# Performance work log

Hardware: AMD Instinct MI355X
Metric: run time of the kernel (lower is better)

The kernel has to match this reference:

```python
import jax, jax.numpy as jnp
import numpy as np

B, NQ, NK = 16, 512, 1024
CQ, CV = 128, 128
H, D = 8, 64            # nb_heads, attention_size
SCALE = float(np.sqrt(D))


def setup_inputs() -> dict:
    key = jax.random.key(0)
    ks = jax.random.split(key, 10)
    s = 0.02
    return {
        "query": jax.random.normal(ks[0], (B, NQ, CQ), jnp.float32),
        "key": jax.random.normal(ks[1], (B, NK, CV), jnp.float32),
        "c_mask": jax.random.randint(ks[2], (B, NK), 0, 2).astype(jnp.float32),
        # torch Linear params, stored as [in, out] so y = x @ W + b
        "Wq": jax.random.normal(ks[3], (CQ, H * D), jnp.float32) * s,
        "bq": jnp.zeros((H * D,), jnp.float32),
        "Wk": jax.random.normal(ks[4], (CV, H * D), jnp.float32) * s,
        "bk": jnp.zeros((H * D,), jnp.float32),
        "Wv": jax.random.normal(ks[5], (CV, H * D), jnp.float32) * s,
        "bv": jnp.zeros((H * D,), jnp.float32),
    }


def reference(query, key, c_mask, Wq, bq, Wk, bk, Wv, bv):
    # projections -> [B, N, H, D]
    q = (query @ Wq + bq).reshape(B, NQ, H, D)
    k = (key @ Wk + bk).reshape(B, NK, H, D)
    v = (key @ Wv + bv).reshape(B, NK, H, D)
    # scaled scores [B, H, NQ, NK]
    scores = jnp.einsum('bqhd,bkhd->bhqk', q / SCALE, k)
    # additive mask: c_mask [B, NK] broadcasts over heads and queries
    scores = scores - 100000.0 * (1.0 - c_mask[:, None, None, :])
    attn = jax.nn.softmax(scores, axis=-1)
    # weighted values -> [B, NQ, H, D] -> concat heads
    c = jnp.einsum('bhqk,bkhd->bqhd', attn, v)
    return c.reshape(B, NQ, H * D)
```

## Files before the change

kernel.cpp:

```cpp
#include <hip/hip_runtime.h>
#include <hip/hip_bf16.h>

#define B_  16
#define NQ_ 512
#define NK_ 1024
#define CQ_ 128
#define H_  8
#define D_  64
#define HD_ 512

typedef __attribute__((ext_vector_type(8))) short short8;
typedef __attribute__((ext_vector_type(4))) float floatx4;

__device__ __forceinline__ short f2bf(float f) {
    union { float f; unsigned u; } x; x.f = f;
    unsigned r = (x.u + 0x7fffu + ((x.u >> 16) & 1u)) >> 16;
    return (short)r;
}
__device__ __forceinline__ int f2bf_pk(float a, float b) {
    __hip_bfloat162 h = __float22bfloat162_rn(make_float2(a, b));
    int r; __builtin_memcpy(&r, &h, 4); return r;
}
__device__ __forceinline__ short8 pack8(float4 a, float4 b) {
    union { int4 i; short8 s; } u;
    u.i = make_int4(f2bf_pk(a.x, a.y), f2bf_pk(a.z, a.w),
                    f2bf_pk(b.x, b.y), f2bf_pk(b.z, b.w));
    return u.s;
}
__device__ __forceinline__ int2 packi2(floatx4 a) {
    return make_int2(f2bf_pk(a[0], a[1]), f2bf_pk(a[2], a[3]));
}
__device__ __forceinline__ void async16(const short* g, short* l) {
    __builtin_amdgcn_global_load_lds(
        (const __attribute__((address_space(1))) void*)g,
        (__attribute__((address_space(3))) void*)l, 16, 0, 0);
}

__global__ __launch_bounds__(256) void prep_kernel(
    const float* __restrict__ W0, const float* __restrict__ W1,
    const float* __restrict__ W2, short* __restrict__ T0,
    short* __restrict__ T1, short* __restrict__ T2,
    const float* __restrict__ bq, float* __restrict__ bqs, float qscale,
    const float* __restrict__ cmask, int* __restrict__ idx,
    float* __restrict__ cm2, int* __restrict__ npad)
{
    const int blk = blockIdx.x, t = threadIdx.x;
    if (blk == 48) {
        bqs[t]       = bq[t] * qscale;
        bqs[t + 256] = bq[t + 256] * qscale;
        return;
    }
    if (blk >= 49) {
        __shared__ int wsum[4];
        const int b = blk - 49;
        const int w = t >> 6, lane = t & 63;
        float4 m4 = *(const float4*)(cmask + b * NK_ + t * 4);
        const int m0 = m4.x > 0.5f, m1 = m4.y > 0.5f, m2 = m4.z > 0.5f, m3 = m4.w > 0.5f;
        const int s = m0 + m1 + m2 + m3;
        int v = s;
        #pragma unroll
        for (int off = 1; off < 64; off <<= 1) {
            int u = __shfl_up(v, off);
            if (lane >= off) v += u;
        }
        if (lane == 63) wsum[w] = v;
        __syncthreads();
        int pre = 0;
        #pragma unroll
        for (int i = 0; i < 4; ++i) if (i < w) pre += wsum[i];
        int pos = pre + v - s;
        const int base = b * NK_;
        if (m0) { idx[base + pos] = t * 4 + 0; cm2[base + pos] = 1.0f; ++pos; }
        if (m1) { idx[base + pos] = t * 4 + 1; cm2[base + pos] = 1.0f; ++pos; }
        if (m2) { idx[base + pos] = t * 4 + 2; cm2[base + pos] = 1.0f; ++pos; }
        if (m3) { idx[base + pos] = t * 4 + 3; cm2[base + pos] = 1.0f; ++pos; }
        const int total = wsum[0] + wsum[1] + wsum[2] + wsum[3];
        for (int j = total + t; j < NK_; j += 256) {
            idx[base + j] = 0; cm2[base + j] = 0.0f;
        }
        if (t == 0) npad[b] = (total + 127) & ~127;
        return;
    }
    __shared__ short tsh[32 * 132];
    const int mat = blk >> 4, nb = blk & 15;
    const float* W = mat == 0 ? W0 : (mat == 1 ? W1 : W2);
    short* T = mat == 0 ? T0 : (mat == 1 ? T1 : T2);
    const float s = mat == 0 ? qscale : 1.0f;
    #pragma unroll
    for (int i = 0; i < 4; ++i) {
        const int i2 = i * 256 + t;
        const int k = i2 >> 3, c = (i2 & 7) * 4;
        float4 v = *(const float4*)(W + (size_t)k * HD_ + nb * 32 + c);
        tsh[(c + 0) * 132 + k] = f2bf(v.x * s);
        tsh[(c + 1) * 132 + k] = f2bf(v.y * s);
        tsh[(c + 2) * 132 + k] = f2bf(v.z * s);
        tsh[(c + 3) * 132 + k] = f2bf(v.w * s);
    }
    __syncthreads();
    #pragma unroll
    for (int j = 0; j < 2; ++j) {
        const int i2 = j * 256 + t;
        const int n = i2 >> 4, seg = (i2 & 15) * 8;
        *(short8*)(T + (size_t)(nb * 32 + n) * CQ_ + seg) =
            *(const short8*)&tsh[n * 132 + seg];
    }
}

__global__ __launch_bounds__(256, 4) void kvproj_kernel(
    const float* __restrict__ key_,
    const short* __restrict__ wkt, const short* __restrict__ wvt,
    const float* __restrict__ bk, const float* __restrict__ bv,
    short* __restrict__ ks, short* __restrict__ vt,
    const int* __restrict__ idx, const int* __restrict__ npad)
{
    __shared__ __align__(16) short csh[9216];

    int bx = blockIdx.x;
    const short* Wt; const float* bias; short* out; int transposed;
    if (bx < 128) { Wt = wkt; bias = bk; out = ks; transposed = 0; }
    else { bx -= 128; Wt = wvt; bias = bv; out = vt; transposed = 1; }

    const int mbase = bx * 128;
    const int b  = mbase >> 10;
    const int r0 = mbase & 1023;
    if (r0 >= npad[b]) return;

    const int tid  = threadIdx.x;
    const int w    = tid >> 6, lane = tid & 63;
    const int l15  = lane & 15, quad = lane >> 4;
    const int* ib = idx + b * NK_;

    short8 afr[2][4];
    #pragma unroll
    for (int mt = 0; mt < 2; ++mt) {
        const int krow = ib[r0 + w * 32 + mt * 16 + l15];
        const float* xrow = key_ + (size_t)(b * NK_ + krow) * CQ_;
        #pragma unroll
        for (int kt = 0; kt < 4; ++kt)
            afr[mt][kt] = pack8(*(const float4*)(xrow + kt * 32 + quad * 8),
                                *(const float4*)(xrow + kt * 32 + quad * 8 + 4));
    }

    #pragma unroll
    for (int hh = 0; hh < 2; ++hh) {
        const int h = blockIdx.y * 2 + hh;
        short8 bfr[4][4];
        #pragma unroll
        for (int nt = 0; nt < 4; ++nt) {
            const short8* wrow = (const short8*)(Wt + (size_t)(h * 64 + nt * 16 + l15) * CQ_);
            #pragma unroll
            for (int kt = 0; kt < 4; ++kt) bfr[nt][kt] = wrow[kt * 4 + quad];
        }
        floatx4 acc[2][4];
        #pragma unroll
        for (int mt = 0; mt < 2; ++mt)
            #pragma unroll
            for (int nt = 0; nt < 4; ++nt) {
                floatx4 a = {0.f, 0.f, 0.f, 0.f};
                #pragma unroll
                for (int kt = 0; kt < 4; ++kt)
                    a = __builtin_amdgcn_mfma_f32_16x16x32_bf16(afr[mt][kt], bfr[nt][kt], a, 0, 0, 0);
                acc[mt][nt] = a;
            }
        __syncthreads();
        #pragma unroll
        for (int mt = 0; mt < 2; ++mt)
            #pragma unroll
            for (int nt = 0; nt < 4; ++nt) {
                const float bvv = bias[h * 64 + nt * 16 + l15];
                #pragma unroll
                for (int i = 0; i < 4; ++i) {
                    const short s = f2bf(acc[mt][nt][i] + bvv);
                    const int m = w * 32 + mt * 16 + quad * 4 + i;
                    const int n = nt * 16 + l15;
                    if (!transposed) csh[m * 72 + n]  = s;
                    else             csh[n * 136 + m] = s;
                }
            }
        __syncthreads();

        const size_t bh = (size_t)(b * H_ + h);
        if (!transposed) {
            short* dst = out + (bh * NK_ + r0) * D_;
            #pragma unroll
            for (int it = 0; it < 4; ++it) {
                const int i2 = it * 256 + tid;
                const int row = i2 >> 3, c8 = (i2 & 7) * 8;
                *(short8*)(dst + i2 * 8) = *(const short8*)&csh[row * 72 + c8];
            }
        } else {
            short* dst = out + bh * D_ * NK_ + r0;
            #pragma unroll
            for (int it = 0; it < 4; ++it) {
                const int i2 = it * 256 + tid;
                const int row = i2 >> 4, c8 = (i2 & 15) * 8;
                *(short8*)(dst + (size_t)row * NK_ + c8) = *(const short8*)&csh[row * 136 + c8];
            }
        }
    }
}

__global__ __launch_bounds__(256, 4) void attn_kernel(
    const float* __restrict__ query, const short* __restrict__ ks,
    const short* __restrict__ vt, const float* __restrict__ cm2,
    const short* __restrict__ wqt, const float* __restrict__ bqs,
    const int* __restrict__ npad, float* __restrict__ out)
{
    __shared__ __align__(16) short kbuf[2][64 * 64];
    __shared__ __align__(16) short vbuf[2][64 * 64];
    __shared__ __align__(16) short psh[64 * 64];

    const int tid = threadIdx.x;
    const int w = tid >> 6, lane = tid & 63;
    const int l15 = lane & 15, quad = lane >> 4;

    const int bx   = blockIdx.x;
    const int bh_i = bx & 127;
    const int qq   = bx >> 7;
    const int h    = bh_i & 7;
    const int b    = bh_i >> 3;

    const size_t bh = (size_t)bh_i;
    const short* kb_ = ks + bh * NK_ * D_;
    const short* vb  = vt + bh * D_ * NK_;
    const float* mk  = cm2 + (size_t)b * NK_;
    const int nc = npad[b] >> 6;

    const int prow = w * 16 + l15;

    short8 qa[2];
    {
        short8 waf[4][4];
        #pragma unroll
        for (int dt = 0; dt < 4; ++dt)
            #pragma unroll
            for (int kt = 0; kt < 4; ++kt)
                waf[dt][kt] = *(const short8*)(wqt + (size_t)(h * 64 + dt * 16 + l15) * CQ_ + kt * 32 + quad * 8);
        const float* qrow = query + ((size_t)b * NQ_ + qq * 64 + prow) * CQ_;
        short8 bqf[4];
        #pragma unroll
        for (int kt = 0; kt < 4; ++kt)
            bqf[kt] = pack8(*(const float4*)(qrow + kt * 32 + quad * 8),
                            *(const float4*)(qrow + kt * 32 + quad * 8 + 4));
        #pragma unroll
        for (int dt = 0; dt < 4; ++dt) {
            float4 bi = *(const float4*)(bqs + h * 64 + dt * 16 + quad * 4);
            floatx4 a = {bi.x, bi.y, bi.z, bi.w};
            #pragma unroll
            for (int kt = 0; kt < 4; ++kt)
                a = __builtin_amdgcn_mfma_f32_16x16x32_bf16(waf[dt][kt], bqf[kt], a, 0, 0, 0);
            const int c16 = (dt * 2 + (quad >> 1)) ^ (prow & 7);
            *(int2*)&psh[prow * 64 + c16 * 8 + (quad & 1) * 4] = packi2(a);
        }
        qa[0] = *(const short8*)&psh[prow * 64 + ((quad    ) ^ (prow & 7)) * 8];
        qa[1] = *(const short8*)&psh[prow * 64 + ((4 + quad) ^ (prow & 7)) * 8];
    }

    const int srow8 = lane >> 3, sc = lane & 7;
    auto stage = [&](int kb0, short* kdst, short* vdst) {
        #pragma unroll
        for (int j = 0; j < 2; ++j) {
            const int row = w * 16 + j * 8 + srow8;
            const int cs = sc ^ (row & 7);
            async16(kb_ + (size_t)(kb0 + row) * D_ + cs * 8, &kdst[(w * 16 + j * 8) * 64]);
            async16(vb + (size_t)row * NK_ + kb0 + cs * 8, &vdst[(w * 16 + j * 8) * 64]);
        }
    };

    float l_lane = 0.f;
    floatx4 o_acc[4];
    #pragma unroll
    for (int dt = 0; dt < 4; ++dt) o_acc[dt] = (floatx4){0.f, 0.f, 0.f, 0.f};

    stage(0, kbuf[0], vbuf[0]);
    __syncthreads();

    for (int t = 0; t < nc; ++t) {
        const int cur = t & 1;
        if (t + 1 < nc) stage((t + 1) * 64, kbuf[cur ^ 1], vbuf[cur ^ 1]);
        const short* kb  = kbuf[cur];
        const short* vbl = vbuf[cur];
        const int kbase = t * 64;

        short8 ka[4][2];
        #pragma unroll
        for (int nt = 0; nt < 4; ++nt) {
            const int row = nt * 16 + l15;
            ka[nt][0] = *(const short8*)&kb[row * 64 + ((quad    ) ^ (row & 7)) * 8];
            ka[nt][1] = *(const short8*)&kb[row * 64 + ((4 + quad) ^ (row & 7)) * 8];
        }
        short8 vf[2][4];
        #pragma unroll
        for (int dt = 0; dt < 4; ++dt) {
            const int row = dt * 16 + l15;
            vf[0][dt] = *(const short8*)&vbl[row * 64 + ((quad    ) ^ (row & 7)) * 8];
            vf[1][dt] = *(const short8*)&vbl[row * 64 + ((4 + quad) ^ (row & 7)) * 8];
        }
        float4 m4[4];
        #pragma unroll
        for (int nt = 0; nt < 4; ++nt)
            m4[nt] = *(const float4*)(mk + kbase + nt * 16 + quad * 4);

        floatx4 st[4];
        #pragma unroll
        for (int nt = 0; nt < 4; ++nt) {
            floatx4 a = {0.f, 0.f, 0.f, 0.f};
            a = __builtin_amdgcn_mfma_f32_16x16x32_bf16(ka[nt][1], qa[1], a, 0, 0, 0);
            a = __builtin_amdgcn_mfma_f32_16x16x32_bf16(ka[nt][0], qa[0], a, 0, 0, 0);
            st[nt] = a;
        }
        float psum = 0.f;
        #pragma unroll
        for (int nt = 0; nt < 4; ++nt) {
            float p0 = m4[nt].x * __builtin_amdgcn_exp2f(st[nt][0]);
            float p1 = m4[nt].y * __builtin_amdgcn_exp2f(st[nt][1]);
            float p2 = m4[nt].z * __builtin_amdgcn_exp2f(st[nt][2]);
            float p3 = m4[nt].w * __builtin_amdgcn_exp2f(st[nt][3]);
            psum += (p0 + p1) + (p2 + p3);
            int2 pk = make_int2(f2bf_pk(p0, p1), f2bf_pk(p2, p3));
            const int c16 = (2 * nt + (quad >> 1)) ^ (prow & 7);
            *(int2*)&psh[prow * 64 + c16 * 8 + (quad & 1) * 4] = pk;
        }
        l_lane += psum;
        #pragma unroll
        for (int kt = 0; kt < 2; ++kt) {
            short8 pa = *(const short8*)&psh[prow * 64 + ((kt * 4 + quad) ^ (prow & 7)) * 8];
            #pragma unroll
            for (int dt = 0; dt < 4; ++dt)
                o_acc[dt] = __builtin_amdgcn_mfma_f32_16x16x32_bf16(vf[kt][dt], pa, o_acc[dt], 0, 0, 0);
        }
        __syncthreads();
    }

    {
        float ls = l_lane;
        ls += __shfl_xor(ls, 16);
        ls += __shfl_xor(ls, 32);
        const float linv = 1.0f / ls;
        const int qr = qq * 64 + prow;
        float* orow = out + ((size_t)b * NQ_ + qr) * HD_ + h * D_;
        #pragma unroll
        for (int dt = 0; dt < 4; ++dt) {
            float4 v = make_float4(o_acc[dt][0] * linv, o_acc[dt][1] * linv,
                                   o_acc[dt][2] * linv, o_acc[dt][3] * linv);
            *(float4*)(orow + dt * 16 + quad * 4) = v;
        }
    }
}

extern "C" void kernel_launch(void* const* d_in, const int* in_sizes, int n_in,
                              void* d_out, int out_size, void* d_ws, size_t ws_size,
                              hipStream_t stream) {
    const float* query = (const float*)d_in[0];
    const float* key   = (const float*)d_in[1];
    const float* cmask = (const float*)d_in[2];
    const float* Wq    = (const float*)d_in[3];
    const float* bq    = (const float*)d_in[4];
    const float* Wk    = (const float*)d_in[5];
    const float* bk    = (const float*)d_in[6];
    const float* Wv    = (const float*)d_in[7];
    const float* bv    = (const float*)d_in[8];
    float* out = (float*)d_out;

    char* ws = (char*)d_ws;
    short* ks  = (short*)(ws);
    short* vt  = (short*)(ws + (size_t)(16u << 20));
    char*  w32 = ws + (size_t)(32u << 20);
    short* wqt = (short*)(w32);
    short* wkt = (short*)(w32 + 131072);
    short* wvt = (short*)(w32 + 131072 * 2);
    float* bqs = (float*)(w32 + 131072 * 3);
    int*   idx = (int*)(w32 + 131072 * 3 + 4096);
    float* cm2 = (float*)(w32 + 131072 * 3 + 4096 + 65536);
    int*  npad = (int*)(w32 + 131072 * 3 + 4096 + 131072);

    const float qscale = 0.125f * 1.44269504f;
    prep_kernel<<<dim3(65), dim3(256), 0, stream>>>(
        Wq, Wk, Wv, wqt, wkt, wvt, bq, bqs, qscale, cmask, idx, cm2, npad);

    kvproj_kernel<<<dim3(256, 4), dim3(256), 0, stream>>>(
        key, wkt, wvt, bk, bv, ks, vt, idx, npad);

    attn_kernel<<<dim3(1024), dim3(256), 0, stream>>>(
        query, ks, vt, cm2, wqt, bqs, npad, out);
}
```

Before: 139.7 us.

## Fuse K/V projection and attention into one kernel with atomic-flag dependencies

Result: slower. 222.9 us (+59.6%).

```diff
diff --git a/kernel.cpp b/kernel.cpp
--- a/kernel.cpp
+++ b/kernel.cpp
@@ -106,244 +106,260 @@
     }
 }
 
-__global__ __launch_bounds__(256, 4) void kvproj_kernel(
-    const float* __restrict__ key_,
-    const short* __restrict__ wkt, const short* __restrict__ wvt,
-    const float* __restrict__ bk, const float* __restrict__ bv,
-    short* __restrict__ ks, short* __restrict__ vt,
-    const int* __restrict__ idx, const int* __restrict__ npad)
+__global__ __launch_bounds__(256, 4) void kvattn_kernel(
+    const float* __restrict__ query, const float* __restrict__ key_,
+    const short* __restrict__ wqt, const short* __restrict__ wkt,
+    const short* __restrict__ wvt, const float* __restrict__ bk,
+    const float* __restrict__ bv, const float* __restrict__ bqs,
+    const int* __restrict__ idx, const float* __restrict__ cm2,
+    const int* __restrict__ npad, short* __restrict__ ks,
+    short* __restrict__ vt, unsigned* __restrict__ flags,
+    float* __restrict__ out)
 {
-    __shared__ __align__(16) short csh[9216];
-
-    int bx = blockIdx.x;
-    const short* Wt; const float* bias; short* out; int transposed;
-    if (bx < 128) { Wt = wkt; bias = bk; out = ks; transposed = 0; }
-    else { bx -= 128; Wt = wvt; bias = bv; out = vt; transposed = 1; }
-
-    const int mbase = bx * 128;
-    const int b  = mbase >> 10;
-    const int r0 = mbase & 1023;
-    if (r0 >= npad[b]) return;
-
-    const int tid  = threadIdx.x;
-    const int w    = tid >> 6, lane = tid & 63;
-    const int l15  = lane & 15, quad = lane >> 4;
-    const int* ib = idx + b * NK_;
-
-    short8 afr[2][4];
-    #pragma unroll
-    for (int mt = 0; mt < 2; ++mt) {
-        const int krow = ib[r0 + w * 32 + mt * 16 + l15];
-        const float* xrow = key_ + (size_t)(b * NK_ + krow) * CQ_;
-        #pragma unroll
-        for (int kt = 0; kt < 4; ++kt)
-            afr[mt][kt] = pack8(*(const float4*)(xrow + kt * 32 + quad * 8),
-                                *(const float4*)(xrow + kt * 32 + quad * 8 + 4));
-    }
-
-    #pragma unroll
-    for (int hh = 0; hh < 2; ++hh) {
-        const int h = blockIdx.y * 2 + hh;
-        short8 bfr[4][4];
-        #pragma unroll
-        for (int nt = 0; nt < 4; ++nt) {
-            const short8* wrow = (const short8*)(Wt + (size_t)(h * 64 + nt * 16 + l15) * CQ_);
-            #pragma unroll
-            for (int kt = 0; kt < 4; ++kt) bfr[nt][kt] = wrow[kt * 4 + quad];
-        }
-        floatx4 acc[2][4];
-        #pragma unroll
-        for (int mt = 0; mt < 2; ++mt)
-            #pragma unroll
-            for (int nt = 0; nt < 4; ++nt) {
-                floatx4 a = {0.f, 0.f, 0.f, 0.f};
-                #pragma unroll
-                for (int kt = 0; kt < 4; ++kt)
-                    a = __builtin_amdgcn_mfma_f32_16x16x32_bf16(afr[mt][kt], bfr[nt][kt], a, 0, 0, 0);
-                acc[mt][nt] = a;
-            }
-        __syncthreads();
-        #pragma unroll
-        for (int mt = 0; mt < 2; ++mt)
-            #pragma unroll
-            for (int nt = 0; nt < 4; ++nt) {
-                const float bvv = bias[h * 64 + nt * 16 + l15];
-                #pragma unroll
-                for (int i = 0; i < 4; ++i) {
-                    const short s = f2bf(acc[mt][nt][i] + bvv);
-                    const int m = w * 32 + mt * 16 + quad * 4 + i;
-                    const int n = nt * 16 + l15;
-                    if (!transposed) csh[m * 72 + n]  = s;
-                    else             csh[n * 136 + m] = s;
-                }
-            }
-        __syncthreads();
-
-        const size_t bh = (size_t)(b * H_ + h);
-        if (!transposed) {
-            short* dst = out + (bh * NK_ + r0) * D_;
-            #pragma unroll
-            for (int it = 0; it < 4; ++it) {
-                const int i2 = it * 256 + tid;
-                const int row = i2 >> 3, c8 = (i2 & 7) * 8;
-                *(short8*)(dst + i2 * 8) = *(const short8*)&csh[row * 72 + c8];
-            }
-        } else {
-            short* dst = out + bh * D_ * NK_ + r0;
-            #pragma unroll
-            for (int it = 0; it < 4; ++it) {
-                const int i2 = it * 256 + tid;
-                const int row = i2 >> 4, c8 = (i2 & 15) * 8;
-                *(short8*)(dst + (size_t)row * NK_ + c8) = *(const short8*)&csh[row * 136 + c8];
-            }
-        }
-    }
-}
-
-__global__ __launch_bounds__(256, 4) void attn_kernel(
-    const float* __restrict__ query, const short* __restrict__ ks,
-    const short* __restrict__ vt, const float* __restrict__ cm2,
-    const short* __restrict__ wqt, const float* __restrict__ bqs,
-    const int* __restrict__ npad, float* __restrict__ out)
-{
-    __shared__ __align__(16) short kbuf[2][64 * 64];
-    __shared__ __align__(16) short vbuf[2][64 * 64];
-    __shared__ __align__(16) short psh[64 * 64];
-
+    __shared__ __align__(16) char smem[40960];
     const int tid = threadIdx.x;
     const int w = tid >> 6, lane = tid & 63;
     const int l15 = lane & 15, quad = lane >> 4;
 
-    const int bx   = blockIdx.x;
-    const int bh_i = bx & 127;
-    const int qq   = bx >> 7;
-    const int h    = bh_i & 7;
-    const int b    = bh_i >> 3;
-
-    const size_t bh = (size_t)bh_i;
-    const short* kb_ = ks + bh * NK_ * D_;
-    const short* vb  = vt + bh * D_ * NK_;
-    const float* mk  = cm2 + (size_t)b * NK_;
-    const int nc = npad[b] >> 6;
-
-    const int prow = w * 16 + l15;
-
-    short8 qa[2];
     {
-        short8 waf[4][4];
+        int bx = blockIdx.x & 255;
+        const int y = blockIdx.x >> 8;
+        const short* Wt; const float* bias; short* op; int transposed;
+        if (bx < 128) { Wt = wkt; bias = bk; op = ks; transposed = 0; }
+        else { bx -= 128; Wt = wvt; bias = bv; op = vt; transposed = 1; }
+
+        const int mbase = bx * 128;
+        const int b  = mbase >> 10;
+        const int r0 = mbase & 1023;
+        if (r0 < npad[b]) {
+            short* csh = (short*)smem;
+            const int* ib = idx + b * NK_;
+
+            short8 afr[2][4];
+            #pragma unroll
+            for (int mt = 0; mt < 2; ++mt) {
+                const int krow = ib[r0 + w * 32 + mt * 16 + l15];
+                const float* xrow = key_ + (size_t)(b * NK_ + krow) * CQ_;
+                #pragma unroll
+                for (int kt = 0; kt < 4; ++kt)
+                    afr[mt][kt] = pack8(*(const float4*)(xrow + kt * 32 + quad * 8),
+                                        *(const float4*)(xrow + kt * 32 + quad * 8 + 4));
+            }
+
+            #pragma unroll
+            for (int hh = 0; hh < 2; ++hh) {
+                const int h = y * 2 + hh;
+                short8 bfr[4][4];
+                #pragma unroll
+                for (int nt = 0; nt < 4; ++nt) {
+                    const short8* wrow = (const short8*)(Wt + (size_t)(h * 64 + nt * 16 + l15) * CQ_);
+                    #pragma unroll
+                    for (int kt = 0; kt < 4; ++kt) bfr[nt][kt] = wrow[kt * 4 + quad];
+                }
+                floatx4 acc[2][4];
+                #pragma unroll
+                for (int mt = 0; mt < 2; ++mt)
+                    #pragma unroll
+                    for (int nt = 0; nt < 4; ++nt) {
+                        floatx4 a = {0.f, 0.f, 0.f, 0.f};
+                        #pragma unroll
+                        for (int kt = 0; kt < 4; ++kt)
+                            a = __builtin_amdgcn_mfma_f32_16x16x32_bf16(afr[mt][kt], bfr[nt][kt], a, 0, 0, 0);
+                        acc[mt][nt] = a;
+                    }
+                __syncthreads();
+                #pragma unroll
+                for (int mt = 0; mt < 2; ++mt)
+                    #pragma unroll
+                    for (int nt = 0; nt < 4; ++nt) {
+                        const float bvv = bias[h * 64 + nt * 16 + l15];
+                        #pragma unroll
+                        for (int i = 0; i < 4; ++i) {
+                            const short sv = f2bf(acc[mt][nt][i] + bvv);
+                            const int m = w * 32 + mt * 16 + quad * 4 + i;
+                            const int n = nt * 16 + l15;
+                            if (!transposed) csh[m * 72 + n]  = sv;
+                            else             csh[n * 136 + m] = sv;
+                        }
+                    }
+                __syncthreads();
+
+                const size_t bh = (size_t)(b * H_ + h);
+                if (!transposed) {
+                    short* dst = op + (bh * NK_ + r0) * D_;
+                    #pragma unroll
+                    for (int it = 0; it < 4; ++it) {
+                        const int i2 = it * 256 + tid;
+                        const int row = i2 >> 3, c8 = (i2 & 7) * 8;
+                        *(short8*)(dst + i2 * 8) = *(const short8*)&csh[row * 72 + c8];
+                    }
+                } else {
+                    short* dst = op + bh * D_ * NK_ + r0;
+                    #pragma unroll
+                    for (int it = 0; it < 4; ++it) {
+                        const int i2 = it * 256 + tid;
+                        const int row = i2 >> 4, c8 = (i2 & 15) * 8;
+                        *(short8*)(dst + (size_t)row * NK_ + c8) = *(const short8*)&csh[row * 136 + c8];
+                    }
+                }
+            }
+            __syncthreads();
+        }
+        if (tid == 0) {
+            __threadfence();
+            atomicAdd(&flags[(b * 4 + y) * 2 + transposed], 1u);
+        }
+    }
+
+    {
+        short* const kbuf0 = (short*)smem;
+        short* const vbuf0 = (short*)smem + 8192;
+        short* const psh   = (short*)smem + 16384;
+
+        const int bx   = blockIdx.x;
+        const int bh_i = bx & 127;
+        const int qq   = bx >> 7;
+        const int h    = bh_i & 7;
+        const int b    = bh_i >> 3;
+
+        const size_t bh = (size_t)bh_i;
+        const short* kb_ = ks + bh * NK_ * D_;
+        const short* vb  = vt + bh * D_ * NK_;
+        const float* mk  = cm2 + (size_t)b * NK_;
+        const int nc = npad[b] >> 6;
+
+        const int prow = w * 16 + l15;
+
+        short8 qa[2];
+        {
+            short8 waf[4][4];
+            #pragma unroll
+            for (int dt = 0; dt < 4; ++dt)
+                #pragma unroll
+                for (int kt = 0; kt < 4; ++kt)
+                    waf[dt][kt] = *(const short8*)(wqt + (size_t)(h * 64 + dt * 16 + l15) * CQ_ + kt * 32 + quad * 8);
+            const float* qrow = query + ((size_t)b * NQ_ + qq * 64 + prow) * CQ_;
+            short8 bqf[4];
+            #pragma unroll
+            for (int kt = 0; kt < 4; ++kt)
+                bqf[kt] = pack8(*(const float4*)(qrow + kt * 32 + quad * 8),
+                                *(const float4*)(qrow + kt * 32 + quad * 8 + 4));
+            #pragma unroll
+            for (int dt = 0; dt < 4; ++dt) {
+                float4 bi = *(const float4*)(bqs + h * 64 + dt * 16 + quad * 4);
+                floatx4 a = {bi.x, bi.y, bi.z, bi.w};
+                #pragma unroll
+                for (int kt = 0; kt < 4; ++kt)
+                    a = __builtin_amdgcn_mfma_f32_16x16x32_bf16(waf[dt][kt], bqf[kt], a, 0, 0, 0);
+                const int c16 = (dt * 2 + (quad >> 1)) ^ (prow & 7);
+                *(int2*)&psh[prow * 64 + c16 * 8 + (quad & 1) * 4] = packi2(a);
+            }
+            qa[0] = *(const short8*)&psh[prow * 64 + ((quad    ) ^ (prow & 7)) * 8];
+            qa[1] = *(const short8*)&psh[prow * 64 + ((4 + quad) ^ (prow & 7)) * 8];
+        }
+
+        if (tid == 0) {
+            unsigned* fk = &flags[(b * 4 + (h >> 1)) * 2 + 0];
+            unsigned* fv = &flags[(b * 4 + (h >> 1)) * 2 + 1];
+            long long t0 = clock64();
+            while (__hip_atomic_load(fk, __ATOMIC_RELAXED, __HIP_MEMORY_SCOPE_AGENT) < 8u ||
+                   __hip_atomic_load(fv, __ATOMIC_RELAXED, __HIP_MEMORY_SCOPE_AGENT) < 8u) {
+                __builtin_amdgcn_s_sleep(8);
+                if (clock64() - t0 > (1ll << 30)) break;
+            }
+            __threadfence();
+        }
+        __syncthreads();
+
+        const int srow8 = lane >> 3, sc = lane & 7;
+        auto stage = [&](int kb0, short* kdst, short* vdst) {
+            #pragma unroll
+            for (int j = 0; j < 2; ++j) {
+                const int row = w * 16 + j * 8 + srow8;
+                const int cs = sc ^ (row & 7);
+                async16(kb_ + (size_t)(kb0 + row) * D_ + cs * 8, &kdst[(w * 16 + j * 8) * 64]);
+                async16(vb + (size_t)row * NK_ + kb0 + cs * 8, &vdst[(w * 16 + j * 8) * 64]);
+            }
+        };
+
+        float l_lane = 0.f;
+        floatx4 o_acc[4];
         #pragma unroll
-        for (int dt = 0; dt < 4; ++dt)
-            #pragma unroll
-            for (int kt = 0; kt < 4; ++kt)
-                waf[dt][kt] = *(const short8*)(wqt + (size_t)(h * 64 + dt * 16 + l15) * CQ_ + kt * 32 + quad * 8);
-        const float* qrow = query + ((size_t)b * NQ_ + qq * 64 + prow) * CQ_;
-        short8 bqf[4];
-        #pragma unroll
-        for (int kt = 0; kt < 4; ++kt)
-            bqf[kt] = pack8(*(const float4*)(qrow + kt * 32 + quad * 8),
-                            *(const float4*)(qrow + kt * 32 + quad * 8 + 4));
-        #pragma unroll
-        for (int dt = 0; dt < 4; ++dt) {
-            float4 bi = *(const float4*)(bqs + h * 64 + dt * 16 + quad * 4);
-            floatx4 a = {bi.x, bi.y, bi.z, bi.w};
-            #pragma unroll
-            for (int kt = 0; kt < 4; ++kt)
-                a = __builtin_amdgcn_mfma_f32_16x16x32_bf16(waf[dt][kt], bqf[kt], a, 0, 0, 0);
-            const int c16 = (dt * 2 + (quad >> 1)) ^ (prow & 7);
-            *(int2*)&psh[prow * 64 + c16 * 8 + (quad & 1) * 4] = packi2(a);
-        }
-        qa[0] = *(const short8*)&psh[prow * 64 + ((quad    ) ^ (prow & 7)) * 8];
-        qa[1] = *(const short8*)&psh[prow * 64 + ((4 + quad) ^ (prow & 7)) * 8];
-    }
-
-    const int srow8 = lane >> 3, sc = lane & 7;
-    auto stage = [&](int kb0, short* kdst, short* vdst) {
-        #pragma unroll
-        for (int j = 0; j < 2; ++j) {
-            const int row = w * 16 + j * 8 + srow8;
-            const int cs = sc ^ (row & 7);
-            async16(kb_ + (size_t)(kb0 + row) * D_ + cs * 8, &kdst[(w * 16 + j * 8) * 64]);
-            async16(vb + (size_t)row * NK_ + kb0 + cs * 8, &vdst[(w * 16 + j * 8) * 64]);
-        }
-    };
-
-    float l_lane = 0.f;
-    floatx4 o_acc[4];
-    #pragma unroll
-    for (int dt = 0; dt < 4; ++dt) o_acc[dt] = (floatx4){0.f, 0.f, 0.f, 0.f};
-
-    stage(0, kbuf[0], vbuf[0]);
-    __syncthreads();
-
-    for (int t = 0; t < nc; ++t) {
-        const int cur = t & 1;
-        if (t + 1 < nc) stage((t + 1) * 64, kbuf[cur ^ 1], vbuf[cur ^ 1]);
-        const short* kb  = kbuf[cur];
-        const short* vbl = vbuf[cur];
-        const int kbase = t * 64;
-
-        short8 ka[4][2];
-        #pragma unroll
-        for (int nt = 0; nt < 4; ++nt) {
-            const int row = nt * 16 + l15;
-            ka[nt][0] = *(const short8*)&kb[row * 64 + ((quad    ) ^ (row & 7)) * 8];
-            ka[nt][1] = *(const short8*)&kb[row * 64 + ((4 + quad) ^ (row & 7)) * 8];
-        }
-        short8 vf[2][4];
-        #pragma unroll
-        for (int dt = 0; dt < 4; ++dt) {
-            const int row = dt * 16 + l15;
-            vf[0][dt] = *(const short8*)&vbl[row * 64 + ((quad    ) ^ (row & 7)) * 8];
-            vf[1][dt] = *(const short8*)&vbl[row * 64 + ((4 + quad) ^ (row & 7)) * 8];
-        }
-        float4 m4[4];
-        #pragma unroll
-        for (int nt = 0; nt < 4; ++nt)
-            m4[nt] = *(const float4*)(mk + kbase + nt * 16 + quad * 4);
-
-        floatx4 st[4];
-        #pragma unroll
-        for (int nt = 0; nt < 4; ++nt) {
-            floatx4 a = {0.f, 0.f, 0.f, 0.f};
-            a = __builtin_amdgcn_mfma_f32_16x16x32_bf16(ka[nt][1], qa[1], a, 0, 0, 0);
-            a = __builtin_amdgcn_mfma_f32_16x16x32_bf16(ka[nt][0], qa[0], a, 0, 0, 0);
-            st[nt] = a;
-        }
-        float psum = 0.f;
-        #pragma unroll
-        for (int nt = 0; nt < 4; ++nt) {
-            float p0 = m4[nt].x * __builtin_amdgcn_exp2f(st[nt][0]);
-            float p1 = m4[nt].y * __builtin_amdgcn_exp2f(st[nt][1]);
-            float p2 = m4[nt].z * __builtin_amdgcn_exp2f(st[nt][2]);
-            float p3 = m4[nt].w * __builtin_amdgcn_exp2f(st[nt][3]);
-            psum += (p0 + p1) + (p2 + p3);
-            int2 pk = make_int2(f2bf_pk(p0, p1), f2bf_pk(p2, p3));
-            const int c16 = (2 * nt + (quad >> 1)) ^ (prow & 7);
-            *(int2*)&psh[prow * 64 + c16 * 8 + (quad & 1) * 4] = pk;
-        }
-        l_lane += psum;
-        #pragma unroll
-        for (int kt = 0; kt < 2; ++kt) {
-            short8 pa = *(const short8*)&psh[prow * 64 + ((kt * 4 + quad) ^ (prow & 7)) * 8];
-            #pragma unroll
-            for (int dt = 0; dt < 4; ++dt)
-                o_acc[dt] = __builtin_amdgcn_mfma_f32_16x16x32_bf16(vf[kt][dt], pa, o_acc[dt], 0, 0, 0);
-        }
+        for (int dt = 0; dt < 4; ++dt) o_acc[dt] = (floatx4){0.f, 0.f, 0.f, 0.f};
+
+        stage(0, kbuf0, vbuf0);
         __syncthreads();
-    }
-
-    {
-        float ls = l_lane;
-        ls += __shfl_xor(ls, 16);
-        ls += __shfl_xor(ls, 32);
-        const float linv = 1.0f / ls;
-        const int qr = qq * 64 + prow;
-        float* orow = out + ((size_t)b * NQ_ + qr) * HD_ + h * D_;
-        #pragma unroll
-        for (int dt = 0; dt < 4; ++dt) {
-            float4 v = make_float4(o_acc[dt][0] * linv, o_acc[dt][1] * linv,
-                                   o_acc[dt][2] * linv, o_acc[dt][3] * linv);
-            *(float4*)(orow + dt * 16 + quad * 4) = v;
+
+        for (int t = 0; t < nc; ++t) {
+            const int cur = t & 1;
+            if (t + 1 < nc) stage((t + 1) * 64, kbuf0 + (cur ^ 1) * 4096, vbuf0 + (cur ^ 1) * 4096);
+            const short* kb  = kbuf0 + cur * 4096;
+            const short* vbl = vbuf0 + cur * 4096;
+            const int kbase = t * 64;
+
+            short8 ka[4][2];
+            #pragma unroll
+            for (int nt = 0; nt < 4; ++nt) {
+                const int row = nt * 16 + l15;
+                ka[nt][0] = *(const short8*)&kb[row * 64 + ((quad    ) ^ (row & 7)) * 8];
+                ka[nt][1] = *(const short8*)&kb[row * 64 + ((4 + quad) ^ (row & 7)) * 8];
+            }
+            short8 vf[2][4];
+            #pragma unroll
+            for (int dt = 0; dt < 4; ++dt) {
+                const int row = dt * 16 + l15;
+                vf[0][dt] = *(const short8*)&vbl[row * 64 + ((quad    ) ^ (row & 7)) * 8];
+                vf[1][dt] = *(const short8*)&vbl[row * 64 + ((4 + quad) ^ (row & 7)) * 8];
+            }
+            float4 m4[4];
+            #pragma unroll
+            for (int nt = 0; nt < 4; ++nt)
+                m4[nt] = *(const float4*)(mk + kbase + nt * 16 + quad * 4);
+
+            floatx4 st[4];
+            #pragma unroll
+            for (int nt = 0; nt < 4; ++nt) {
+                floatx4 a = {0.f, 0.f, 0.f, 0.f};
+                a = __builtin_amdgcn_mfma_f32_16x16x32_bf16(ka[nt][1], qa[1], a, 0, 0, 0);
+                a = __builtin_amdgcn_mfma_f32_16x16x32_bf16(ka[nt][0], qa[0], a, 0, 0, 0);
+                st[nt] = a;
+            }
+            float psum = 0.f;
+            #pragma unroll
+            for (int nt = 0; nt < 4; ++nt) {
+                float p0 = m4[nt].x * __builtin_amdgcn_exp2f(st[nt][0]);
+                float p1 = m4[nt].y * __builtin_amdgcn_exp2f(st[nt][1]);
+                float p2 = m4[nt].z * __builtin_amdgcn_exp2f(st[nt][2]);
+                float p3 = m4[nt].w * __builtin_amdgcn_exp2f(st[nt][3]);
+                psum += (p0 + p1) + (p2 + p3);
+                int2 pk = make_int2(f2bf_pk(p0, p1), f2bf_pk(p2, p3));
+                const int c16 = (2 * nt + (quad >> 1)) ^ (prow & 7);
+                *(int2*)&psh[prow * 64 + c16 * 8 + (quad & 1) * 4] = pk;
+            }
+            l_lane += psum;
+            #pragma unroll
+            for (int kt = 0; kt < 2; ++kt) {
+                short8 pa = *(const short8*)&psh[prow * 64 + ((kt * 4 + quad) ^ (prow & 7)) * 8];
+                #pragma unroll
+                for (int dt = 0; dt < 4; ++dt)
+                    o_acc[dt] = __builtin_amdgcn_mfma_f32_16x16x32_bf16(vf[kt][dt], pa, o_acc[dt], 0, 0, 0);
+            }
+            __syncthreads();
+        }
+
+        {
+            float ls = l_lane;
+            ls += __shfl_xor(ls, 16);
+            ls += __shfl_xor(ls, 32);
+            const float linv = 1.0f / ls;
+            const int qr = qq * 64 + prow;
+            float* orow = out + ((size_t)b * NQ_ + qr) * HD_ + h * D_;
+            #pragma unroll
+            for (int dt = 0; dt < 4; ++dt) {
+                float4 v = make_float4(o_acc[dt][0] * linv, o_acc[dt][1] * linv,
+                                       o_acc[dt][2] * linv, o_acc[dt][3] * linv);
+                *(float4*)(orow + dt * 16 + quad * 4) = v;
+            }
         }
     }
 }
@@ -373,14 +389,15 @@
     int*   idx = (int*)(w32 + 131072 * 3 + 4096);
     float* cm2 = (float*)(w32 + 131072 * 3 + 4096 + 65536);
     int*  npad = (int*)(w32 + 131072 * 3 + 4096 + 131072);
+    unsigned* flags = (unsigned*)(w32 + 131072 * 3 + 4096 + 131072 + 1024);
+
+    hipMemsetAsync(flags, 0, 512, stream);
 
     const float qscale = 0.125f * 1.44269504f;
     prep_kernel<<<dim3(65), dim3(256), 0, stream>>>(
         Wq, Wk, Wv, wqt, wkt, wvt, bq, bqs, qscale, cmask, idx, cm2, npad);
 
-    kvproj_kernel<<<dim3(256, 4), dim3(256), 0, stream>>>(
-        key, wkt, wvt, bk, bv, ks, vt, idx, npad);
-
-    attn_kernel<<<dim3(1024), dim3(256), 0, stream>>>(
-        query, ks, vt, cm2, wqt, bqs, npad, out);
-}
+    kvattn_kernel<<<dim3(1024), dim3(256), 0, stream>>>(
+        query, key, wqt, wkt, wvt, bk, bv, bqs, idx, cm2, npad,
+        ks, vt, flags, out);
+}
```
